# Optimization experiments

Hardware: AMD Instinct MI355X
Metric: run time of the kernel (lower is better)

The kernel has to match this reference:

```python
import jax, jax.numpy as jnp
import numpy as np

N_BLADES = 8  # Cl(3,0): 1, e1, e2, e3 and their products (bitmask blade indexing)


def _blade_sign(a: int, b: int) -> int:
    # Sign from reordering basis vectors when multiplying blades a*b (Euclidean metric).
    a >>= 1
    s = 0
    while a:
        s += bin(a & b).count('1')
        a >>= 1
    return -1 if (s & 1) else 1


def make_cayley() -> np.ndarray:
    C = np.zeros((N_BLADES, N_BLADES, N_BLADES), dtype=np.float32)
    for a in range(N_BLADES):
        for b in range(N_BLADES):
            C[a, b, a ^ b] = float(_blade_sign(a, b))
    return C


def setup_inputs() -> dict:
    key = jax.random.key(0)
    k1, k2 = jax.random.split(key)
    B, Cin, Cout = 8192, 256, 256
    scale = 1.0 / np.sqrt(Cin * N_BLADES)
    x = jax.random.normal(k1, (B, Cin, N_BLADES), dtype=jnp.float32)
    weight = jax.random.normal(k2, (Cout, Cin, N_BLADES), dtype=jnp.float32) * scale
    bias = jnp.zeros((Cout, N_BLADES), dtype=jnp.float32)
    cayley = jnp.asarray(make_cayley())
    return {"x": x, "weight": weight, "bias": bias, "cayley": cayley}


def reference(x, weight, bias, cayley):
    # A[b,o,j,k] = sum_i W[o,i,j] * X[b,i,k]  (weight blade j times input blade k)
    A = jnp.einsum('oij,bik->bojk', weight, x)
    # Contract blade pair (j,k) into output blade l via sparse Cayley table.
    out = jnp.einsum('jkl,bojk->bol', cayley, A)
    return out + bias[None, :, :]
```

## Files before the change

### kernel.cpp

```cpp
#include <hip/hip_runtime.h>
#include <stdint.h>
#include <stddef.h>


typedef __bf16 bf16x8  __attribute__((ext_vector_type(8)));
typedef float  f32x4   __attribute__((ext_vector_type(4)));

#define BM 128
#define BN 128
#define BK 32

__device__ __forceinline__ void async_copy16(void* lds_dst, const void* g_src) {
    __builtin_amdgcn_global_load_lds(
        (__attribute__((address_space(1))) void*)g_src,
        (__attribute__((address_space(3))) void*)lds_dst,
        16, 0, 0);
}

__global__ __launch_bounds__(256) void prep_kernel(
    const float* __restrict__ x, __bf16* __restrict__ Xb, long nx,
    const float* __restrict__ W, const float* __restrict__ cayley,
    __bf16* __restrict__ Wt, int Cin, int Cout, int castBlocks)
{
    __shared__ float Cay[512];
    if ((int)blockIdx.x < castBlocks) {
        long i = ((long)blockIdx.x * 256 + threadIdx.x) * 8;
        if (i + 8 <= nx) {
            const f32x4* p = (const f32x4*)(x + i);
            f32x4 v0 = p[0];
            f32x4 v1 = p[1];
            bf16x8 o;
            o[0] = (__bf16)v0[0]; o[1] = (__bf16)v0[1];
            o[2] = (__bf16)v0[2]; o[3] = (__bf16)v0[3];
            o[4] = (__bf16)v1[0]; o[5] = (__bf16)v1[1];
            o[6] = (__bf16)v1[2]; o[7] = (__bf16)v1[3];
            *(bf16x8*)(Xb + i) = o;
        }
        return;
    }
    for (int t = threadIdx.x; t < 512; t += 256) Cay[t] = cayley[t];
    __syncthreads();

    int flat = (blockIdx.x - castBlocks) * 256 + threadIdx.x;
    int total = Cout * 8 * Cin;
    if (flat >= total) return;
    int i = flat % Cin;
    int n = flat / Cin;
    int o = n >> 3, l = n & 7;

    const float* wrow = W + ((size_t)o * Cin + i) * 8;
    float w8[8];
    #pragma unroll
    for (int j = 0; j < 8; ++j) w8[j] = wrow[j];

    bf16x8 outv;
    #pragma unroll
    for (int k = 0; k < 8; ++k) {
        float s = 0.f;
        #pragma unroll
        for (int j = 0; j < 8; ++j) s += Cay[j * 64 + k * 8 + l] * w8[j];
        outv[k] = (__bf16)s;
    }
    *(bf16x8*)(Wt + (size_t)n * (Cin * 8) + i * 8) = outv;
}

__global__ __launch_bounds__(256, 4) void gemm_bt_kernel(
    const __bf16* __restrict__ A,
    const __bf16* __restrict__ Bt,
    const float*  __restrict__ bias,
    float* __restrict__ C,
    int M, int N, int K)
{
    __shared__ __align__(16) __bf16 As0[BM * BK];
    __shared__ __align__(16) __bf16 As1[BM * BK];
    __shared__ __align__(16) __bf16 Bs0[BN * BK];
    __shared__ __align__(16) __bf16 Bs1[BN * BK];

    const int tid  = threadIdx.x;
    const int wave = tid >> 6;
    const int lane = tid & 63;
    const int quad = lane >> 4;
    const int l16  = lane & 15;

    const int bid   = blockIdx.x;
    const int band  = (bid & 7) | ((bid >> 7) << 3);
    const int ncol  = (bid >> 3) & 15;
    const int mBase = band * BM;
    const int nBase = ncol * BN;

    const int srow = lane >> 2;
    const int sgrp = (lane & 3) ^ ((srow >> 1) & 3);

    const __bf16* gA0 = A  + (size_t)(mBase + (2 * wave + 0) * 16 + srow) * K + sgrp * 8;
    const __bf16* gA1 = A  + (size_t)(mBase + (2 * wave + 1) * 16 + srow) * K + sgrp * 8;
    const __bf16* gB0 = Bt + (size_t)(nBase + (2 * wave + 0) * 16 + srow) * K + sgrp * 8;
    const __bf16* gB1 = Bt + (size_t)(nBase + (2 * wave + 1) * 16 + srow) * K + sgrp * 8;
    const int cOff0 = (2 * wave + 0) * 512;
    const int cOff1 = (2 * wave + 1) * 512;

    const int wm = (wave >> 1) * 64;
    const int wn = (wave & 1) * 64;
    const int offq = (quad ^ ((l16 >> 1) & 3)) * 8;
    const int rowA = (wm + l16) * BK;
    const int rowB = (wn + l16) * BK;

    f32x4 acc[4][4] = {};

#define PREFETCH(BUFA, BUFB, KOFF)                       \
    do {                                                 \
        async_copy16(&BUFA[cOff0], gA0 + (KOFF));        \
        async_copy16(&BUFA[cOff1], gA1 + (KOFF));        \
        async_copy16(&BUFB[cOff0], gB0 + (KOFF));        \
        async_copy16(&BUFB[cOff1], gB1 + (KOFF));        \
    } while (0)

#define COMPUTE(BUFA, BUFB)                                               \
    do {                                                                  \
        const __bf16* fA = &BUFA[rowA] + offq;                            \
        const __bf16* fB = &BUFB[rowB] + offq;                            \
        bf16x8 af[4], bfr[4];                                             \
        _Pragma("unroll")                                                 \
        for (int mt = 0; mt < 4; ++mt)                                    \
            af[mt] = *(const bf16x8*)(fA + mt * 16 * BK);                 \
        _Pragma("unroll")                                                 \
        for (int nt = 0; nt < 4; ++nt)                                    \
            bfr[nt] = *(const bf16x8*)(fB + nt * 16 * BK);                \
        _Pragma("unroll")                                                 \
        for (int mt = 0; mt < 4; ++mt)                                    \
            _Pragma("unroll")                                             \
            for (int nt = 0; nt < 4; ++nt)                                \
                acc[mt][nt] = __builtin_amdgcn_mfma_f32_16x16x32_bf16(    \
                    af[mt], bfr[nt], acc[mt][nt], 0, 0, 0);               \
    } while (0)

    PREFETCH(As0, Bs0, 0);

    int k0 = 0;
    for (; k0 < K - 2 * BK; k0 += 2 * BK) {
        __syncthreads();
        PREFETCH(As1, Bs1, k0 + BK);
        COMPUTE(As0, Bs0);

        __syncthreads();
        PREFETCH(As0, Bs0, k0 + 2 * BK);
        COMPUTE(As1, Bs1);
    }

    __syncthreads();
    PREFETCH(As1, Bs1, k0 + BK);
    COMPUTE(As0, Bs0);

    __syncthreads();
    COMPUTE(As1, Bs1);

#undef PREFETCH
#undef COMPUTE

    float bv[4];
    #pragma unroll
    for (int nt = 0; nt < 4; ++nt)
        bv[nt] = bias[nBase + wn + nt * 16 + l16];

    #pragma unroll
    for (int mt = 0; mt < 4; ++mt) {
        #pragma unroll
        for (int nt = 0; nt < 4; ++nt) {
            const int col = nBase + wn + nt * 16 + l16;
            #pragma unroll
            for (int r = 0; r < 4; ++r) {
                const int row = mBase + wm + mt * 16 + quad * 4 + r;
                C[(size_t)row * N + col] = acc[mt][nt][r] + bv[nt];
            }
        }
    }
}

extern "C" void kernel_launch(void* const* d_in, const int* in_sizes, int n_in,
                              void* d_out, int out_size, void* d_ws, size_t ws_size,
                              hipStream_t stream) {
    const float* x      = (const float*)d_in[0];
    const float* weight = (const float*)d_in[1];
    const float* bias   = (const float*)d_in[2];
    const float* cayley = (const float*)d_in[3];
    float* out = (float*)d_out;

    const int Cout = in_sizes[2] / 8;
    const int Cin  = in_sizes[1] / (Cout * 8);
    const int Bm   = in_sizes[0] / (Cin * 8);
    const int M = Bm;
    const int N = Cout * 8;
    const int K = Cin * 8;

    __bf16* Xb = (__bf16*)d_ws;
    __bf16* Wt = (__bf16*)((char*)d_ws + (size_t)M * K * 2);

    long nx = (long)M * K;
    int castBlocks = (int)(nx / 8 / 256);
    int foldBlocks = (N * Cin + 255) / 256;
    prep_kernel<<<castBlocks + foldBlocks, 256, 0, stream>>>(
        x, Xb, nx, weight, cayley, Wt, Cin, Cout, castBlocks);

    int grid = (M / BM) * (N / BN);
    gemm_bt_kernel<<<grid, 256, 0, stream>>>(Xb, Wt, bias, out, M, N, K);
}
```

Measured before the change: 191.2 us.

## Use 256x256 tiles with 512 threads and a 4-slot async LDS pipeline

Grows the GEMM block tile from 128x128 to 256x256 with 8 waves, each computing 128x64. The double buffer becomes a 4-slot ring with split A/B staging, explicit vmcnt/lgkmcnt waits, raw s_barrier and setprio around MFMA bursts. The aim is more operand reuse per byte loaded and better overlap of global-to-LDS copies with MFMA work. LDS use rises to 128KB per block, limiting occupancy, and the grid shrinks to 256 blocks, which can hurt wave balance across CUs. The block-index mapping and the swizzle formula also change.

Measured after the change: 178.7 us. -6.6%, faster.

```diff
diff --git a/kernel.cpp b/kernel.cpp
--- a/kernel.cpp
+++ b/kernel.cpp
@@ -6,9 +6,11 @@
 typedef __bf16 bf16x8  __attribute__((ext_vector_type(8)));
 typedef float  f32x4   __attribute__((ext_vector_type(4)));
 
-#define BM 128
-#define BN 128
-#define BK 32
+#define BM 256
+#define BN 256
+#define KSLICE 32
+#define NSLICES 64
+#define SLOT_ELEMS (256 * 32)
 
 __device__ __forceinline__ void async_copy16(void* lds_dst, const void* g_src) {
     __builtin_amdgcn_global_load_lds(
@@ -64,17 +66,15 @@
     *(bf16x8*)(Wt + (size_t)n * (Cin * 8) + i * 8) = outv;
 }
 
-__global__ __launch_bounds__(256, 4) void gemm_bt_kernel(
+__global__ __launch_bounds__(512, 2) void gemm_bt_kernel(
     const __bf16* __restrict__ A,
     const __bf16* __restrict__ Bt,
     const float*  __restrict__ bias,
     float* __restrict__ C,
     int M, int N, int K)
 {
-    __shared__ __align__(16) __bf16 As0[BM * BK];
-    __shared__ __align__(16) __bf16 As1[BM * BK];
-    __shared__ __align__(16) __bf16 Bs0[BN * BK];
-    __shared__ __align__(16) __bf16 Bs1[BN * BK];
+    __shared__ __align__(16) __bf16 As[4][SLOT_ELEMS];
+    __shared__ __align__(16) __bf16 Bs[4][SLOT_ELEMS];
 
     const int tid  = threadIdx.x;
     const int wave = tid >> 6;
@@ -82,94 +82,105 @@
     const int quad = lane >> 4;
     const int l16  = lane & 15;
 
-    const int bid   = blockIdx.x;
-    const int band  = (bid & 7) | ((bid >> 7) << 3);
-    const int ncol  = (bid >> 3) & 15;
-    const int mBase = band * BM;
-    const int nBase = ncol * BN;
+    const int bid = blockIdx.x;
+    const int xcd = bid & 7;
+    const int idx = bid >> 3;
+    const int mBase = (xcd * 4 + (idx & 3)) * BM;
+    const int nBase = (idx >> 2) * BN;
 
     const int srow = lane >> 2;
-    const int sgrp = (lane & 3) ^ ((srow >> 1) & 3);
-
-    const __bf16* gA0 = A  + (size_t)(mBase + (2 * wave + 0) * 16 + srow) * K + sgrp * 8;
-    const __bf16* gA1 = A  + (size_t)(mBase + (2 * wave + 1) * 16 + srow) * K + sgrp * 8;
-    const __bf16* gB0 = Bt + (size_t)(nBase + (2 * wave + 0) * 16 + srow) * K + sgrp * 8;
-    const __bf16* gB1 = Bt + (size_t)(nBase + (2 * wave + 1) * 16 + srow) * K + sgrp * 8;
-    const int cOff0 = (2 * wave + 0) * 512;
-    const int cOff1 = (2 * wave + 1) * 512;
-
-    const int wm = (wave >> 1) * 64;
-    const int wn = (wave & 1) * 64;
+    const int sgrp = (lane & 3) ^ ((lane >> 3) & 3);
+    const __bf16* gA0 = A  + (size_t)(mBase + wave * 32 +  0 + srow) * K + sgrp * 8;
+    const __bf16* gA1 = A  + (size_t)(mBase + wave * 32 + 16 + srow) * K + sgrp * 8;
+    const __bf16* gB0 = Bt + (size_t)(nBase + wave * 32 +  0 + srow) * K + sgrp * 8;
+    const __bf16* gB1 = Bt + (size_t)(nBase + wave * 32 + 16 + srow) * K + sgrp * 8;
+    const int stOff = wave * 1024;
+
+#define STAGE_A(slot, q) do {                                          \
+        async_copy16(&As[slot][stOff      ], gA0 + (size_t)(q) * KSLICE); \
+        async_copy16(&As[slot][stOff + 512], gA1 + (size_t)(q) * KSLICE); \
+    } while (0)
+#define STAGE_B(slot, q) do {                                          \
+        async_copy16(&Bs[slot][stOff      ], gB0 + (size_t)(q) * KSLICE); \
+        async_copy16(&Bs[slot][stOff + 512], gB1 + (size_t)(q) * KSLICE); \
+    } while (0)
+
+    const int wm = wave >> 2;
+    const int wn = wave & 3;
     const int offq = (quad ^ ((l16 >> 1) & 3)) * 8;
-    const int rowA = (wm + l16) * BK;
-    const int rowB = (wn + l16) * BK;
-
-    f32x4 acc[4][4] = {};
-
-#define PREFETCH(BUFA, BUFB, KOFF)                       \
-    do {                                                 \
-        async_copy16(&BUFA[cOff0], gA0 + (KOFF));        \
-        async_copy16(&BUFA[cOff1], gA1 + (KOFF));        \
-        async_copy16(&BUFB[cOff0], gB0 + (KOFF));        \
-        async_copy16(&BUFB[cOff1], gB1 + (KOFF));        \
-    } while (0)
-
-#define COMPUTE(BUFA, BUFB)                                               \
-    do {                                                                  \
-        const __bf16* fA = &BUFA[rowA] + offq;                            \
-        const __bf16* fB = &BUFB[rowB] + offq;                            \
-        bf16x8 af[4], bfr[4];                                             \
-        _Pragma("unroll")                                                 \
-        for (int mt = 0; mt < 4; ++mt)                                    \
-            af[mt] = *(const bf16x8*)(fA + mt * 16 * BK);                 \
-        _Pragma("unroll")                                                 \
-        for (int nt = 0; nt < 4; ++nt)                                    \
-            bfr[nt] = *(const bf16x8*)(fB + nt * 16 * BK);                \
-        _Pragma("unroll")                                                 \
-        for (int mt = 0; mt < 4; ++mt)                                    \
-            _Pragma("unroll")                                             \
-            for (int nt = 0; nt < 4; ++nt)                                \
-                acc[mt][nt] = __builtin_amdgcn_mfma_f32_16x16x32_bf16(    \
-                    af[mt], bfr[nt], acc[mt][nt], 0, 0, 0);               \
-    } while (0)
-
-    PREFETCH(As0, Bs0, 0);
-
-    int k0 = 0;
-    for (; k0 < K - 2 * BK; k0 += 2 * BK) {
-        __syncthreads();
-        PREFETCH(As1, Bs1, k0 + BK);
-        COMPUTE(As0, Bs0);
-
-        __syncthreads();
-        PREFETCH(As0, Bs0, k0 + 2 * BK);
-        COMPUTE(As1, Bs1);
-    }
-
+    const int aOff = (wm * 128 + l16) * KSLICE + offq;
+    const int bOff = (wn * 64  + l16) * KSLICE + offq;
+
+    f32x4 acc[8][4] = {};
+
+    STAGE_A(0, 0); STAGE_B(0, 0);
+    STAGE_A(1, 1); STAGE_B(1, 1);
+    STAGE_A(2, 2); STAGE_B(2, 2);
+    STAGE_B(3, 3);
+    asm volatile("s_waitcnt vmcnt(6)" ::: "memory");
     __syncthreads();
-    PREFETCH(As1, Bs1, k0 + BK);
-    COMPUTE(As0, Bs0);
-
-    __syncthreads();
-    COMPUTE(As1, Bs1);
-
-#undef PREFETCH
-#undef COMPUTE
+
+    #pragma unroll 2
+    for (int s = 0; s < NSLICES; ++s) {
+        const __bf16* pa = &As[s & 3][aOff];
+        const __bf16* pb = &Bs[s & 3][bOff];
+
+        bf16x8 af0[4], bf[4];
+        #pragma unroll
+        for (int j = 0; j < 4; ++j) af0[j] = *(const bf16x8*)(pa + j * 512);
+        #pragma unroll
+        for (int n = 0; n < 4; ++n) bf[n]  = *(const bf16x8*)(pb + n * 512);
+        if (s <= 60) STAGE_A((s + 3) & 3, s + 3);
+        __builtin_amdgcn_s_barrier();
+        asm volatile("s_waitcnt lgkmcnt(0)" ::: "memory");
+        __builtin_amdgcn_s_setprio(1);
+        #pragma unroll
+        for (int j = 0; j < 4; ++j)
+            #pragma unroll
+            for (int n = 0; n < 4; ++n)
+                acc[j][n] = __builtin_amdgcn_mfma_f32_16x16x32_bf16(
+                    af0[j], bf[n], acc[j][n], 0, 0, 0);
+        __builtin_amdgcn_s_setprio(0);
+        __builtin_amdgcn_s_barrier();
+
+        bf16x8 af1[4];
+        #pragma unroll
+        for (int j = 0; j < 4; ++j) af1[j] = *(const bf16x8*)(pa + (4 + j) * 512);
+        if (s <= 59) STAGE_B(s & 3, s + 4);
+        __builtin_amdgcn_s_barrier();
+        asm volatile("s_waitcnt lgkmcnt(0)" ::: "memory");
+        __builtin_amdgcn_s_setprio(1);
+        #pragma unroll
+        for (int j = 0; j < 4; ++j)
+            #pragma unroll
+            for (int n = 0; n < 4; ++n)
+                acc[4 + j][n] = __builtin_amdgcn_mfma_f32_16x16x32_bf16(
+                    af1[j], bf[n], acc[4 + j][n], 0, 0, 0);
+        __builtin_amdgcn_s_setprio(0);
+        if (s & 1) {
+            if (s >= 61) asm volatile("s_waitcnt vmcnt(0)" ::: "memory");
+            else         asm volatile("s_waitcnt vmcnt(6)" ::: "memory");
+        }
+        __builtin_amdgcn_s_barrier();
+    }
+
+#undef STAGE_A
+#undef STAGE_B
 
     float bv[4];
     #pragma unroll
-    for (int nt = 0; nt < 4; ++nt)
-        bv[nt] = bias[nBase + wn + nt * 16 + l16];
-
-    #pragma unroll
-    for (int mt = 0; mt < 4; ++mt) {
-        #pragma unroll
-        for (int nt = 0; nt < 4; ++nt) {
-            const int col = nBase + wn + nt * 16 + l16;
+    for (int n = 0; n < 4; ++n)
+        bv[n] = bias[nBase + wn * 64 + n * 16 + l16];
+
+    #pragma unroll
+    for (int m = 0; m < 8; ++m) {
+        #pragma unroll
+        for (int n = 0; n < 4; ++n) {
+            const int col = nBase + wn * 64 + n * 16 + l16;
             #pragma unroll
             for (int r = 0; r < 4; ++r) {
-                const int row = mBase + wm + mt * 16 + quad * 4 + r;
-                C[(size_t)row * N + col] = acc[mt][nt][r] + bv[nt];
+                const int row = mBase + wm * 128 + m * 16 + quad * 4 + r;
+                C[(size_t)row * N + col] = acc[m][n][r] + bv[n];
             }
         }
     }
@@ -201,5 +212,5 @@
         x, Xb, nx, weight, cayley, Wt, Cin, Cout, castBlocks);
 
     int grid = (M / BM) * (N / BN);
-    gemm_bt_kernel<<<grid, 256, 0, stream>>>(Xb, Wt, bias, out, M, N, K);
-}
+    gemm_bt_kernel<<<grid, 512, 0, stream>>>(Xb, Wt, bias, out, M, N, K);
+}
```
